# Kernel tuning notes

Hardware: AMD Instinct MI355X
Metric: run time of the kernel (lower is better)

Reference implementation:

```python
import jax, jax.numpy as jnp
import numpy as np

# Faithful JAX port of the approxmatch algorithm (Fan et al. / PyTorch-EMDLoss CUDA kernel):
# iterative soft bipartite matching with annealed temperature levels -4^j for j=8..-1, then 0,
# tracking remaining capacities ('saturation') of both point sets.

EPS = 1e-9

def _approx_match(xyz1, xyz2):
    # xyz1: [B,N,D], xyz2: [B,M,D] -> match: [B,N,M]
    B, n, _ = xyz1.shape
    m = xyz2.shape[1]
    factorl = max(n, m) // n  # capacity per point in set 1
    factorr = max(n, m) // m  # capacity per point in set 2
    # pairwise squared distances [B,N,M]
    d2 = jnp.sum((xyz1[:, :, None, :] - xyz2[:, None, :, :]) ** 2, axis=-1)
    # annealing levels: -4^8, -4^7, ..., -4^-1, 0
    levels = jnp.array([-(4.0 ** j) for j in range(8, -2, -1)] + [0.0],
                       dtype=xyz1.dtype)
    satl0 = jnp.full((B, n), float(factorl), dtype=xyz1.dtype)
    satr0 = jnp.full((B, m), float(factorr), dtype=xyz1.dtype)
    match0 = jnp.zeros((B, n, m), dtype=xyz1.dtype)

    def step(carry, level):
        satl, satr, match = carry
        # soft assignment weights scaled by remaining capacity of set 2
        w = jnp.exp(level * d2) * satr[:, None, :]                      # [B,N,M]
        # row-normalize, scaled by remaining capacity of set 1
        w = w / (jnp.sum(w, axis=2, keepdims=True) + EPS) * satl[:, :, None]
        # column capacity clipping
        ss = jnp.sum(w, axis=1) + EPS                                   # [B,M]
        r = jnp.minimum(satr / ss, 1.0)
        w = w * r[:, None, :]
        satr = jnp.maximum(satr - jnp.sum(w, axis=1), 0.0)
        satl = jnp.maximum(satl - jnp.sum(w, axis=2), 0.0)
        return (satl, satr, match + w), None

    (_, _, match), _ = jax.lax.scan(step, (satl0, satr0, match0), levels)
    return match


def setup_inputs() -> dict:
    key = jax.random.key(0)
    k1, k2 = jax.random.split(key)
    xyz1 = jax.random.normal(k1, (8, 2048, 3), dtype=jnp.float32)
    xyz2 = jax.random.normal(k2, (8, 2048, 3), dtype=jnp.float32)
    return {"xyz1": xyz1, "xyz2": xyz2}


def reference(xyz1, xyz2):
    # EMD cost per batch element: sum_{k,l} match[k,l] * ||x1_k - x2_l||
    match = _approx_match(xyz1, xyz2)                                   # [B,N,M]
    d = jnp.sqrt(jnp.sum((xyz1[:, :, None, :] - xyz2[:, None, :, :]) ** 2,
                         axis=-1))                                      # [B,N,M]
    return jnp.sum(match * d, axis=(1, 2))                              # [B]
```

## Files before the change

kernel.cpp:

```cpp
#include <hip/hip_runtime.h>
#include <math.h>

typedef float f2 __attribute__((ext_vector_type(2)));

static constexpr int   B_   = 8;
static constexpr int   N_   = 2048;
static constexpr int   TPB  = 256;
static constexpr int   TILE = 16;
static constexpr int   BPB  = 128;
static constexpr int   NBLK = B_ * BPB;
static constexpr int   BN   = B_ * N_;
static constexpr float EPS_ = 1e-9f;
static constexpr float LOG2E = 1.4426950408889634f;

#define WS_X1    (ws)
#define WS_X2    (ws + 4*BN)
#define WS_SATL  (ws + 8*BN)
#define WS_SATR  (ws + 9*BN)
#define WS_SCAL  (ws + 10*BN)
#define WS_LSCAL (ws + 11*BN)
#define WS_LSATR (ws + 12*BN)
#define WS_LWR   (ws + 13*BN)
#define WS_WR    (ws + 14*BN)
#define WS_COST  (ws + 15*BN)

__global__ void __launch_bounds__(TPB)
emd_init(const float* __restrict__ xyz1, const float* __restrict__ xyz2,
         float* __restrict__ ws)
{
    const int idx = blockIdx.x * TPB + threadIdx.x;
    if (idx >= BN) return;
    float x = xyz1[idx*3], y = xyz1[idx*3+1], z = xyz1[idx*3+2];
    reinterpret_cast<float4*>(WS_X1)[idx] =
        make_float4(x, y, z, fmaf(x,x, fmaf(y,y, z*z)));
    x = xyz2[idx*3]; y = xyz2[idx*3+1]; z = xyz2[idx*3+2];
    reinterpret_cast<float4*>(WS_X2)[idx] =
        make_float4(x, y, z, fmaf(x,x, fmaf(y,y, z*z)));
    WS_SATL[idx]  = 1.f;
    WS_SATR[idx]  = 1.f;
    WS_LSATR[idx] = 0.f;
    WS_COST[idx]  = 0.f;
}

template<int NA>
__device__ __forceinline__ void reduce_multi(float* sc, const float (*s)[8],
                                             int t, float* rs)
{
    const int c = t >> 1, g = t & 1;
    __syncthreads();
#pragma unroll
    for (int a = 0; a < NA; ++a) {
        float* red = sc + a * 2176;
#pragma unroll
        for (int j = 0; j < 8; ++j) red[c*17 + g*8 + j] = s[a][j];
    }
    __syncthreads();
    {
        const int col = t & 15, seg = t >> 4;
#pragma unroll
        for (int a = 0; a < NA; ++a) {
            const float* red = sc + a * 2176;
            float v = 0.f;
#pragma unroll
            for (int k = 0; k < 8; ++k) v += red[(seg*8 + k)*17 + col];
            sc[6528 + a*272 + seg*17 + col] = v;
        }
    }
    __syncthreads();
    if (t < 16) {
#pragma unroll
        for (int a = 0; a < NA; ++a) {
            float r = 0.f;
#pragma unroll
            for (int q = 0; q < 16; ++q) r += sc[6528 + a*272 + q*17 + t];
            rs[a] = r;
        }
    }
}

template<int MODE>
__global__ void __launch_bounds__(TPB, 4)
emd_pass(float* __restrict__ ws, float* __restrict__ out,
         const float lvA, const float lvB)
{
    constexpr int SMEM = (MODE == 2) ? 40960 : 32768;
    __shared__ __align__(16) char smem[SMEM];
    float4* pts  = reinterpret_cast<float4*>(smem);
    float*  auxB = reinterpret_cast<float*>(smem + 32768);
    float*  sc   = reinterpret_cast<float*>(smem);

    const int b    = blockIdx.x >> 7;
    const int tile = blockIdx.x & 127;
    const int t    = threadIdx.x;

    const float4* x1v = reinterpret_cast<const float4*>(WS_X1) + b * N_;
    const float4* x2v = reinterpret_cast<const float4*>(WS_X2) + b * N_;
    const float* lscal = WS_LSCAL + b * N_;
    const float* lsatr = WS_LSATR + b * N_;
    const float* lwr   = WS_LWR   + b * N_;
    const float* wrp   = WS_WR    + b * N_;

    for (int p = t; p < N_; p += TPB) {
        if (MODE == 0) {
            float4 v = x2v[p];
            pts[p] = make_float4(v.x, v.y, v.z, lvB * v.w);
        } else if (MODE == 1) {
            float4 v = x1v[p];
            pts[p] = make_float4(v.x, v.y, v.z, fmaf(lvB, v.w, lscal[p]));
        } else if (MODE == 2) {
            float4 v = x2v[p];
            pts[p]  = make_float4(v.x, v.y, v.z, fmaf(lvA, v.w, lwr[p]));
            auxB[p] = fmaf(lvB, v.w, lsatr[p]);
        } else {
            float4 v = x2v[p];
            pts[p] = make_float4(v.x, v.y, v.z, wrp[p]);
        }
    }

    const float4* ownv = (MODE == 1) ? x2v : x1v;
    const int ob = tile * TILE + (t & 1) * 8;
    f2 kx[4], ky[4], kz[4], kc[4];
#pragma unroll
    for (int jp = 0; jp < 4; ++jp) {
        float4 v0 = ownv[ob + 2*jp], v1 = ownv[ob + 2*jp + 1];
        if (MODE == 0 || MODE == 1) {
            const float m2 = -2.f * lvB;
            kx[jp] = (f2){m2*v0.x, m2*v1.x};
            ky[jp] = (f2){m2*v0.y, m2*v1.y};
            kz[jp] = (f2){m2*v0.z, m2*v1.z};
            kc[jp] = (f2){lvB*v0.w, lvB*v1.w};
        } else {
            kx[jp] = (f2){-2.f*v0.x, -2.f*v1.x};
            ky[jp] = (f2){-2.f*v0.y, -2.f*v1.y};
            kz[jp] = (f2){-2.f*v0.z, -2.f*v1.z};
            kc[jp] = (f2){v0.w, v1.w};
        }
    }
    __syncthreads();

    float s1[8], s2[8], s3[8];
#pragma unroll
    for (int j = 0; j < 8; ++j) { s1[j] = 0.f; s2[j] = 0.f; s3[j] = 0.f; }

    int l = t >> 1;
    float4 p = pts[l];
    float  ab = (MODE == 2) ? auxB[l] : 0.f;

#pragma unroll 2
    for (int i = 0; i < 16; ++i) {
        const int ln = (l + 128) & (N_ - 1);
        const float4 pn = pts[ln];
        float abn = 0.f;
        if (MODE == 2) abn = auxB[ln];

        const f2 px = (f2){p.x, p.x}, py = (f2){p.y, p.y}, pz = (f2){p.z, p.z};
        float p2s = 0.f;
        if (MODE == 2 || MODE == 3)
            p2s = fmaf(p.x, p.x, fmaf(p.y, p.y, p.z * p.z));

#pragma unroll
        for (int jp = 0; jp < 4; ++jp) {
            if (MODE == 0 || MODE == 1) {
                f2 a = kc[jp] + (f2){p.w, p.w};
                a = kz[jp] * pz + a;
                a = ky[jp] * py + a;
                a = kx[jp] * px + a;
                s1[2*jp]   += __builtin_amdgcn_exp2f(a.x);
                s1[2*jp+1] += __builtin_amdgcn_exp2f(a.y);
            } else if (MODE == 2) {
                f2 dq = kz[jp] * pz + kc[jp];
                dq = ky[jp] * py + dq;
                dq = kx[jp] * px + dq;
                const float d20 = dq.x + p2s, d21 = dq.y + p2s;
                const float sq0 = __builtin_amdgcn_sqrtf(fmaxf(d20, 0.f));
                const float sq1 = __builtin_amdgcn_sqrtf(fmaxf(d21, 0.f));
                const float eA0 = __builtin_amdgcn_exp2f(fmaf(lvA, dq.x, p.w));
                const float eA1 = __builtin_amdgcn_exp2f(fmaf(lvA, dq.y, p.w));
                const float eB0 = __builtin_amdgcn_exp2f(fmaf(lvB, dq.x, ab));
                const float eB1 = __builtin_amdgcn_exp2f(fmaf(lvB, dq.y, ab));
                s1[2*jp]   += eA0;            s1[2*jp+1] += eA1;
                s2[2*jp]    = fmaf(eA0, sq0, s2[2*jp]);
                s2[2*jp+1]  = fmaf(eA1, sq1, s2[2*jp+1]);
                s3[2*jp]   += eB0;            s3[2*jp+1] += eB1;
            } else {
                f2 dq = kz[jp] * pz + kc[jp];
                dq = ky[jp] * py + dq;
                dq = kx[jp] * px + dq;
                const float sq0 = __builtin_amdgcn_sqrtf(fmaxf(dq.x + p2s, 0.f));
                const float sq1 = __builtin_amdgcn_sqrtf(fmaxf(dq.y + p2s, 0.f));
                s2[2*jp]   = fmaf(p.w, sq0, s2[2*jp]);
                s2[2*jp+1] = fmaf(p.w, sq1, s2[2*jp+1]);
            }
        }
        p = pn; ab = abn; l = ln;
    }

    const int gidx = b * N_ + tile * TILE + t;

    if (MODE == 0) {
        float rs[1];
        reduce_multi<1>(sc, &s1, t, rs);
        if (t < TILE) {
            const float scv = WS_SATL[gidx] / (rs[0] + EPS_);
            WS_SCAL[gidx]  = scv;
            WS_LSCAL[gidx] = __log2f(scv);
        }
    } else if (MODE == 1) {
        float rs[1];
        reduce_multi<1>(sc, &s1, t, rs);
        if (t < TILE) {
            const float sr  = WS_SATR[gidx];
            const float w1s = sr * rs[0];
            const float rr  = fminf(sr / (w1s + EPS_), 1.f);
            const float wrv = sr * rr;
            const float srn = fmaxf(sr - rr * w1s, 0.f);
            WS_SATR[gidx]  = srn;
            WS_WR[gidx]    = wrv;
            WS_LWR[gidx]   = __log2f(wrv);
            WS_LSATR[gidx] = __log2f(srn);
        }
    } else if (MODE == 2) {
        float sall[3][8];
#pragma unroll
        for (int j = 0; j < 8; ++j) {
            sall[0][j] = s1[j]; sall[1][j] = s2[j]; sall[2][j] = s3[j];
        }
        float rs[3];
        reduce_multi<3>(sc, sall, t, rs);
        if (t < TILE) {
            const float scp = WS_SCAL[gidx];
            const float sln = fmaxf(WS_SATL[gidx] - scp * rs[0], 0.f);
            WS_COST[gidx]   = fmaf(scp, rs[1], WS_COST[gidx]);
            const float scn = sln / (rs[2] + EPS_);
            WS_SATL[gidx]  = sln;
            WS_SCAL[gidx]  = scn;
            WS_LSCAL[gidx] = __log2f(scn);
        }
    } else {
        float rs[1];
        reduce_multi<1>(sc, &s2, t, rs);
        if (t < 16) {
            float v = fmaf(WS_SCAL[gidx], rs[0], WS_COST[gidx]);
#pragma unroll
            for (int k = 8; k >= 1; k >>= 1) v += __shfl_xor(v, k, 16);
            if (t == 0) atomicAdd(out + b, v);
        }
    }
}

extern "C" void kernel_launch(void* const* d_in, const int* in_sizes, int n_in,
                              void* d_out, int out_size, void* d_ws, size_t ws_size,
                              hipStream_t stream)
{
    const float* xyz1 = (const float*)d_in[0];
    const float* xyz2 = (const float*)d_in[1];
    float* out = (float*)d_out;
    float* ws  = (float*)d_ws;

    hipMemsetAsync(d_out, 0, B_ * sizeof(float), stream);
    emd_init<<<BN / TPB, TPB, 0, stream>>>(xyz1, xyz2, ws);

    static const float levels[11] = {
        -65536.f, -16384.f, -4096.f, -1024.f, -256.f,
        -64.f, -16.f, -4.f, -1.f, -0.25f, 0.f};

    emd_pass<0><<<NBLK, TPB, 0, stream>>>(ws, out, 0.f, levels[0] * LOG2E);
    emd_pass<1><<<NBLK, TPB, 0, stream>>>(ws, out, 0.f, levels[0] * LOG2E);
    for (int lev = 1; lev < 11; ++lev) {
        emd_pass<2><<<NBLK, TPB, 0, stream>>>(ws, out, levels[lev-1] * LOG2E,
                                                       levels[lev]   * LOG2E);
        emd_pass<1><<<NBLK, TPB, 0, stream>>>(ws, out, 0.f, levels[lev] * LOG2E);
    }
    emd_pass<3><<<NBLK, TPB, 0, stream>>>(ws, out, 0.f, 0.f);
}
```

Baseline: 320.5 us.

## Use 1024-thread blocks with 32-row tiles and shuffle-based reductions

```diff
diff --git a/kernel.cpp b/kernel.cpp
--- a/kernel.cpp
+++ b/kernel.cpp
@@ -5,10 +5,9 @@
 
 static constexpr int   B_   = 8;
 static constexpr int   N_   = 2048;
-static constexpr int   TPB  = 256;
-static constexpr int   TILE = 16;
-static constexpr int   BPB  = 128;
-static constexpr int   NBLK = B_ * BPB;
+static constexpr int   TPB  = 1024;
+static constexpr int   TILE = 32;
+static constexpr int   NBLK = 512;
 static constexpr int   BN   = B_ * N_;
 static constexpr float EPS_ = 1e-9f;
 static constexpr float LOG2E = 1.4426950408889634f;
@@ -24,11 +23,11 @@
 #define WS_WR    (ws + 14*BN)
 #define WS_COST  (ws + 15*BN)
 
-__global__ void __launch_bounds__(TPB)
+__global__ void __launch_bounds__(256)
 emd_init(const float* __restrict__ xyz1, const float* __restrict__ xyz2,
          float* __restrict__ ws)
 {
-    const int idx = blockIdx.x * TPB + threadIdx.x;
+    const int idx = blockIdx.x * 256 + threadIdx.x;
     if (idx >= BN) return;
     float x = xyz1[idx*3], y = xyz1[idx*3+1], z = xyz1[idx*3+2];
     reinterpret_cast<float4*>(WS_X1)[idx] =
@@ -42,56 +41,128 @@
     WS_COST[idx]  = 0.f;
 }
 
-template<int NA>
-__device__ __forceinline__ void reduce_multi(float* sc, const float (*s)[8],
-                                             int t, float* rs)
-{
-    const int c = t >> 1, g = t & 1;
-    __syncthreads();
-#pragma unroll
-    for (int a = 0; a < NA; ++a) {
-        float* red = sc + a * 2176;
-#pragma unroll
-        for (int j = 0; j < 8; ++j) red[c*17 + g*8 + j] = s[a][j];
-    }
-    __syncthreads();
-    {
-        const int col = t & 15, seg = t >> 4;
-#pragma unroll
-        for (int a = 0; a < NA; ++a) {
-            const float* red = sc + a * 2176;
-            float v = 0.f;
-#pragma unroll
-            for (int k = 0; k < 8; ++k) v += red[(seg*8 + k)*17 + col];
-            sc[6528 + a*272 + seg*17 + col] = v;
-        }
-    }
-    __syncthreads();
-    if (t < 16) {
-#pragma unroll
-        for (int a = 0; a < NA; ++a) {
-            float r = 0.f;
-#pragma unroll
-            for (int q = 0; q < 16; ++q) r += sc[6528 + a*272 + q*17 + t];
-            rs[a] = r;
-        }
+__device__ __forceinline__ void wave_reduce8(float (&s)[8], float* sc, int a,
+                                             int t)
+{
+#pragma unroll
+    for (int j = 0; j < 8; ++j) {
+        float v = s[j];
+        v += __shfl_xor(v, 4, 64);
+        v += __shfl_xor(v, 8, 64);
+        v += __shfl_xor(v, 16, 64);
+        v += __shfl_xor(v, 32, 64);
+        s[j] = v;
+    }
+    const int lane = t & 63, w = t >> 6;
+    if (lane < 4) {
+#pragma unroll
+        for (int j = 0; j < 8; ++j)
+            sc[a*512 + (lane*8 + j)*16 + w] = s[j];
+    }
+}
+
+__device__ __forceinline__ void sweep01(const float4* pts,
+    const f2 (&kx)[4], const f2 (&ky)[4], const f2 (&kz)[4], const f2 (&kc)[4],
+    int t, float (&s1)[8])
+{
+#pragma unroll
+    for (int j = 0; j < 8; ++j) s1[j] = 0.f;
+    int l = t >> 2;
+    float4 p = pts[l];
+#pragma unroll 4
+    for (int i = 0; i < 8; ++i) {
+        const int ln = (l + 256) & (N_ - 1);
+        const float4 pn = pts[ln];
+        const f2 px = (f2){p.x,p.x}, py = (f2){p.y,p.y}, pz = (f2){p.z,p.z};
+        const f2 pw = (f2){p.w,p.w};
+#pragma unroll
+        for (int jp = 0; jp < 4; ++jp) {
+            f2 a = kc[jp] + pw;
+            a = kz[jp] * pz + a;
+            a = ky[jp] * py + a;
+            a = kx[jp] * px + a;
+            s1[2*jp]   += __builtin_amdgcn_exp2f(a.x);
+            s1[2*jp+1] += __builtin_amdgcn_exp2f(a.y);
+        }
+        p = pn; l = ln;
+    }
+}
+
+__device__ __forceinline__ void sweep2(const float4* pts, const float* auxB,
+    const f2 (&kx)[4], const f2 (&ky)[4], const f2 (&kz)[4], const f2 (&kc)[4],
+    float lvA, float lvB, int t, float (&s1)[8], float (&s2)[8], float (&s3)[8])
+{
+#pragma unroll
+    for (int j = 0; j < 8; ++j) { s1[j] = 0.f; s2[j] = 0.f; s3[j] = 0.f; }
+    int l = t >> 2;
+    float4 p = pts[l];
+    float  ab = auxB[l];
+#pragma unroll 2
+    for (int i = 0; i < 8; ++i) {
+        const int ln = (l + 256) & (N_ - 1);
+        const float4 pn = pts[ln];
+        const float  abn = auxB[ln];
+        const f2 px = (f2){p.x,p.x}, py = (f2){p.y,p.y}, pz = (f2){p.z,p.z};
+        const float p2s = fmaf(p.x, p.x, fmaf(p.y, p.y, p.z * p.z));
+#pragma unroll
+        for (int jp = 0; jp < 4; ++jp) {
+            f2 dq = kz[jp] * pz + kc[jp];
+            dq = ky[jp] * py + dq;
+            dq = kx[jp] * px + dq;
+            const float sq0 = __builtin_amdgcn_sqrtf(fmaxf(dq.x + p2s, 0.f));
+            const float sq1 = __builtin_amdgcn_sqrtf(fmaxf(dq.y + p2s, 0.f));
+            const float eA0 = __builtin_amdgcn_exp2f(fmaf(lvA, dq.x, p.w));
+            const float eA1 = __builtin_amdgcn_exp2f(fmaf(lvA, dq.y, p.w));
+            const float eB0 = __builtin_amdgcn_exp2f(fmaf(lvB, dq.x, ab));
+            const float eB1 = __builtin_amdgcn_exp2f(fmaf(lvB, dq.y, ab));
+            s1[2*jp]   += eA0;            s1[2*jp+1] += eA1;
+            s2[2*jp]    = fmaf(eA0, sq0, s2[2*jp]);
+            s2[2*jp+1]  = fmaf(eA1, sq1, s2[2*jp+1]);
+            s3[2*jp]   += eB0;            s3[2*jp+1] += eB1;
+        }
+        p = pn; ab = abn; l = ln;
+    }
+}
+
+__device__ __forceinline__ void sweep3(const float4* pts,
+    const f2 (&kx)[4], const f2 (&ky)[4], const f2 (&kz)[4],
+    int t, float (&s2)[8])
+{
+#pragma unroll
+    for (int j = 0; j < 8; ++j) s2[j] = 0.f;
+    int l = t >> 2;
+    float4 p = pts[l];
+#pragma unroll 4
+    for (int i = 0; i < 8; ++i) {
+        const int ln = (l + 256) & (N_ - 1);
+        const float4 pn = pts[ln];
+#pragma unroll
+        for (int jp = 0; jp < 4; ++jp) {
+            const float dx0 = p.x - kx[jp].x, dy0 = p.y - ky[jp].x,
+                        dz0 = p.z - kz[jp].x;
+            const float dx1 = p.x - kx[jp].y, dy1 = p.y - ky[jp].y,
+                        dz1 = p.z - kz[jp].y;
+            const float d20 = fmaf(dx0,dx0, fmaf(dy0,dy0, dz0*dz0));
+            const float d21 = fmaf(dx1,dx1, fmaf(dy1,dy1, dz1*dz1));
+            s2[2*jp]   = fmaf(p.w, __builtin_amdgcn_sqrtf(fmaxf(d20,0.f)), s2[2*jp]);
+            s2[2*jp+1] = fmaf(p.w, __builtin_amdgcn_sqrtf(fmaxf(d21,0.f)), s2[2*jp+1]);
+        }
+        p = pn; l = ln;
     }
 }
 
 template<int MODE>
-__global__ void __launch_bounds__(TPB, 4)
+__global__ void __launch_bounds__(TPB, 8)
 emd_pass(float* __restrict__ ws, float* __restrict__ out,
          const float lvA, const float lvB)
 {
-    constexpr int SMEM = (MODE == 2) ? 40960 : 32768;
-    __shared__ __align__(16) char smem[SMEM];
-    float4* pts  = reinterpret_cast<float4*>(smem);
-    float*  auxB = reinterpret_cast<float*>(smem + 32768);
-    float*  sc   = reinterpret_cast<float*>(smem);
-
-    const int b    = blockIdx.x >> 7;
-    const int tile = blockIdx.x & 127;
+    __shared__ __align__(16) float4 pts[N_];
+    __shared__ float aux[N_];
+
+    const int b    = blockIdx.x & 7;
+    const int tile = blockIdx.x >> 3;
     const int t    = threadIdx.x;
+    const int rg   = t & 3;
 
     const float4* x1v = reinterpret_cast<const float4*>(WS_X1) + b * N_;
     const float4* x2v = reinterpret_cast<const float4*>(WS_X2) + b * N_;
@@ -109,8 +180,8 @@
             pts[p] = make_float4(v.x, v.y, v.z, fmaf(lvB, v.w, lscal[p]));
         } else if (MODE == 2) {
             float4 v = x2v[p];
-            pts[p]  = make_float4(v.x, v.y, v.z, fmaf(lvA, v.w, lwr[p]));
-            auxB[p] = fmaf(lvB, v.w, lsatr[p]);
+            pts[p] = make_float4(v.x, v.y, v.z, fmaf(lvA, v.w, lwr[p]));
+            aux[p] = fmaf(lvB, v.w, lsatr[p]);
         } else {
             float4 v = x2v[p];
             pts[p] = make_float4(v.x, v.y, v.z, wrp[p]);
@@ -118,7 +189,7 @@
     }
 
     const float4* ownv = (MODE == 1) ? x2v : x1v;
-    const int ob = tile * TILE + (t & 1) * 8;
+    const int ob = tile * TILE + rg * 8;
     f2 kx[4], ky[4], kz[4], kc[4];
 #pragma unroll
     for (int jp = 0; jp < 4; ++jp) {
@@ -129,88 +200,57 @@
             ky[jp] = (f2){m2*v0.y, m2*v1.y};
             kz[jp] = (f2){m2*v0.z, m2*v1.z};
             kc[jp] = (f2){lvB*v0.w, lvB*v1.w};
-        } else {
+        } else if (MODE == 2) {
             kx[jp] = (f2){-2.f*v0.x, -2.f*v1.x};
             ky[jp] = (f2){-2.f*v0.y, -2.f*v1.y};
             kz[jp] = (f2){-2.f*v0.z, -2.f*v1.z};
             kc[jp] = (f2){v0.w, v1.w};
+        } else {
+            kx[jp] = (f2){v0.x, v1.x};
+            ky[jp] = (f2){v0.y, v1.y};
+            kz[jp] = (f2){v0.z, v1.z};
+            kc[jp] = (f2){0.f, 0.f};
         }
     }
     __syncthreads();
 
     float s1[8], s2[8], s3[8];
-#pragma unroll
-    for (int j = 0; j < 8; ++j) { s1[j] = 0.f; s2[j] = 0.f; s3[j] = 0.f; }
-
-    int l = t >> 1;
-    float4 p = pts[l];
-    float  ab = (MODE == 2) ? auxB[l] : 0.f;
-
-#pragma unroll 2
-    for (int i = 0; i < 16; ++i) {
-        const int ln = (l + 128) & (N_ - 1);
-        const float4 pn = pts[ln];
-        float abn = 0.f;
-        if (MODE == 2) abn = auxB[ln];
-
-        const f2 px = (f2){p.x, p.x}, py = (f2){p.y, p.y}, pz = (f2){p.z, p.z};
-        float p2s = 0.f;
-        if (MODE == 2 || MODE == 3)
-            p2s = fmaf(p.x, p.x, fmaf(p.y, p.y, p.z * p.z));
-
-#pragma unroll
-        for (int jp = 0; jp < 4; ++jp) {
-            if (MODE == 0 || MODE == 1) {
-                f2 a = kc[jp] + (f2){p.w, p.w};
-                a = kz[jp] * pz + a;
-                a = ky[jp] * py + a;
-                a = kx[jp] * px + a;
-                s1[2*jp]   += __builtin_amdgcn_exp2f(a.x);
-                s1[2*jp+1] += __builtin_amdgcn_exp2f(a.y);
-            } else if (MODE == 2) {
-                f2 dq = kz[jp] * pz + kc[jp];
-                dq = ky[jp] * py + dq;
-                dq = kx[jp] * px + dq;
-                const float d20 = dq.x + p2s, d21 = dq.y + p2s;
-                const float sq0 = __builtin_amdgcn_sqrtf(fmaxf(d20, 0.f));
-                const float sq1 = __builtin_amdgcn_sqrtf(fmaxf(d21, 0.f));
-                const float eA0 = __builtin_amdgcn_exp2f(fmaf(lvA, dq.x, p.w));
-                const float eA1 = __builtin_amdgcn_exp2f(fmaf(lvA, dq.y, p.w));
-                const float eB0 = __builtin_amdgcn_exp2f(fmaf(lvB, dq.x, ab));
-                const float eB1 = __builtin_amdgcn_exp2f(fmaf(lvB, dq.y, ab));
-                s1[2*jp]   += eA0;            s1[2*jp+1] += eA1;
-                s2[2*jp]    = fmaf(eA0, sq0, s2[2*jp]);
-                s2[2*jp+1]  = fmaf(eA1, sq1, s2[2*jp+1]);
-                s3[2*jp]   += eB0;            s3[2*jp+1] += eB1;
-            } else {
-                f2 dq = kz[jp] * pz + kc[jp];
-                dq = ky[jp] * py + dq;
-                dq = kx[jp] * px + dq;
-                const float sq0 = __builtin_amdgcn_sqrtf(fmaxf(dq.x + p2s, 0.f));
-                const float sq1 = __builtin_amdgcn_sqrtf(fmaxf(dq.y + p2s, 0.f));
-                s2[2*jp]   = fmaf(p.w, sq0, s2[2*jp]);
-                s2[2*jp+1] = fmaf(p.w, sq1, s2[2*jp+1]);
-            }
-        }
-        p = pn; ab = abn; l = ln;
-    }
+    if (MODE == 0 || MODE == 1) sweep01(pts, kx, ky, kz, kc, t, s1);
+    else if (MODE == 2) sweep2(pts, aux, kx, ky, kz, kc, lvA, lvB, t, s1, s2, s3);
+    else                sweep3(pts, kx, ky, kz, t, s2);
+
+    __syncthreads();
+
+    if (MODE == 2) {
+        wave_reduce8(s1, aux, 0, t);
+        wave_reduce8(s2, aux, 1, t);
+        wave_reduce8(s3, aux, 2, t);
+    } else if (MODE == 3) {
+        wave_reduce8(s2, aux, 0, t);
+    } else {
+        wave_reduce8(s1, aux, 0, t);
+    }
+    __syncthreads();
 
     const int gidx = b * N_ + tile * TILE + t;
 
-    if (MODE == 0) {
-        float rs[1];
-        reduce_multi<1>(sc, &s1, t, rs);
-        if (t < TILE) {
-            const float scv = WS_SATL[gidx] / (rs[0] + EPS_);
+    if (t < 32) {
+        float rs1 = 0.f, rs2 = 0.f, rs3 = 0.f;
+#pragma unroll
+        for (int w = 0; w < 16; ++w) rs1 += aux[t*16 + w];
+        if (MODE == 2) {
+#pragma unroll
+            for (int w = 0; w < 16; ++w) rs2 += aux[512 + t*16 + w];
+#pragma unroll
+            for (int w = 0; w < 16; ++w) rs3 += aux[1024 + t*16 + w];
+        }
+        if (MODE == 0) {
+            const float scv = WS_SATL[gidx] / (rs1 + EPS_);
             WS_SCAL[gidx]  = scv;
             WS_LSCAL[gidx] = __log2f(scv);
-        }
-    } else if (MODE == 1) {
-        float rs[1];
-        reduce_multi<1>(sc, &s1, t, rs);
-        if (t < TILE) {
+        } else if (MODE == 1) {
             const float sr  = WS_SATR[gidx];
-            const float w1s = sr * rs[0];
+            const float w1s = sr * rs1;
             const float rr  = fminf(sr / (w1s + EPS_), 1.f);
             const float wrv = sr * rr;
             const float srn = fmaxf(sr - rr * w1s, 0.f);
@@ -218,31 +258,18 @@
             WS_WR[gidx]    = wrv;
             WS_LWR[gidx]   = __log2f(wrv);
             WS_LSATR[gidx] = __log2f(srn);
-        }
-    } else if (MODE == 2) {
-        float sall[3][8];
-#pragma unroll
-        for (int j = 0; j < 8; ++j) {
-            sall[0][j] = s1[j]; sall[1][j] = s2[j]; sall[2][j] = s3[j];
-        }
-        float rs[3];
-        reduce_multi<3>(sc, sall, t, rs);
-        if (t < TILE) {
+        } else if (MODE == 2) {
             const float scp = WS_SCAL[gidx];
-            const float sln = fmaxf(WS_SATL[gidx] - scp * rs[0], 0.f);
-            WS_COST[gidx]   = fmaf(scp, rs[1], WS_COST[gidx]);
-            const float scn = sln / (rs[2] + EPS_);
+            const float sln = fmaxf(WS_SATL[gidx] - scp * rs1, 0.f);
+            WS_COST[gidx]   = fmaf(scp, rs2, WS_COST[gidx]);
+            const float scn = sln / (rs3 + EPS_);
             WS_SATL[gidx]  = sln;
             WS_SCAL[gidx]  = scn;
             WS_LSCAL[gidx] = __log2f(scn);
-        }
-    } else {
-        float rs[1];
-        reduce_multi<1>(sc, &s2, t, rs);
-        if (t < 16) {
-            float v = fmaf(WS_SCAL[gidx], rs[0], WS_COST[gidx]);
-#pragma unroll
-            for (int k = 8; k >= 1; k >>= 1) v += __shfl_xor(v, k, 16);
+        } else {
+            float v = fmaf(WS_SCAL[gidx], rs1, WS_COST[gidx]);
+#pragma unroll
+            for (int k = 16; k >= 1; k >>= 1) v += __shfl_xor(v, k, 32);
             if (t == 0) atomicAdd(out + b, v);
         }
     }
@@ -258,7 +285,7 @@
     float* ws  = (float*)d_ws;
 
     hipMemsetAsync(d_out, 0, B_ * sizeof(float), stream);
-    emd_init<<<BN / TPB, TPB, 0, stream>>>(xyz1, xyz2, ws);
+    emd_init<<<BN / 256, 256, 0, stream>>>(xyz1, xyz2, ws);
 
     static const float levels[11] = {
         -65536.f, -16384.f, -4096.f, -1024.f, -256.f,
```

Result: slower. 903.5 us (+181.9%).
